# Kernel optimization log

Measured on AMD Instinct MI355X. Metric: run time of the kernel, lower is better.

## Reference

```python
import jax, jax.numpy as jnp
import numpy as np

BATCH, SEQ, FEAT, NUM_BINS = 64, 1024, 512, 32


def setup_inputs() -> dict:
    key = jax.random.key(0)
    k1, k2 = jax.random.split(key)
    features = jax.random.normal(k1, (BATCH, SEQ, FEAT), dtype=jnp.float32)
    # buffer: randn(input_dim, num_bins) / sqrt(input_dim)
    random_projection = jax.random.normal(k2, (FEAT, NUM_BINS), dtype=jnp.float32) / np.sqrt(FEAT)
    return {"features": features, "random_projection": random_projection}


def reference(features, random_projection):
    batch, seq, feat = features.shape
    x = features.reshape(-1, feat)  # [N, feat]
    N = x.shape[0]

    # RunningMeanStd.update from fresh state (mean=0, var=1, count=1e-4)
    eps_count = 1e-4
    batch_mean = x.mean(axis=0)
    batch_var = jnp.var(x, axis=0, ddof=1)  # torch.var is unbiased by default
    tot = eps_count + N
    delta = batch_mean  # - 0
    mean = delta * N / tot
    M2 = 1.0 * eps_count + batch_var * N + (delta ** 2) * eps_count * N / tot
    var = M2 / tot
    sigma = jnp.sqrt(var + 1e-8)

    normalized = (x - mean) / sigma
    projected = normalized @ random_projection  # [N, num_bins]
    bits = (projected > 0).astype(jnp.int64)
    pow2 = jnp.left_shift(jnp.int64(1), jnp.arange(NUM_BINS, dtype=jnp.int64))
    keys = (bits * pow2).sum(axis=-1)  # [N], values < 2^32

    # env_indices=None path: env = arange(N) % batch
    env = jnp.arange(N, dtype=jnp.int64) % batch
    combined = jnp.left_shift(env, 32) | keys  # unique (env, key) id

    # running occurrence count of each (env, key) in sample order i=0..N-1
    order = jnp.argsort(combined, stable=True)  # stable: preserves sample order within group
    s = combined[order]
    idx = jnp.arange(N, dtype=jnp.int64)
    is_start = jnp.concatenate([jnp.ones((1,), bool), s[1:] != s[:-1]])
    seg_start = jax.lax.cummax(jnp.where(is_start, idx, 0))
    occ = idx - seg_start + 1  # 1-based occurrence within group
    counts = jnp.zeros((N,), jnp.int64).at[order].set(occ)

    rewards = 1.0 / jnp.sqrt(counts.astype(features.dtype))
    return rewards.reshape(batch, seq, 1)
```

## Files before the change

kernel.cpp:

```cpp
#include <hip/hip_runtime.h>

using u16 = unsigned short;
using u64 = unsigned long long;
typedef short s16x8 __attribute__((ext_vector_type(8)));
typedef _Float16 f16x8 __attribute__((ext_vector_type(8)));
typedef unsigned short u16x4 __attribute__((ext_vector_type(4)));
typedef float f32x4 __attribute__((ext_vector_type(4)));

constexpr int BATCH = 64, SEQ = 1024, FEAT = 512, NBINS = 32;
constexpr int N = BATCH * SEQ;
constexpr int TAB = 131072;
constexpr unsigned TABMASK = TAB - 1;
constexpr u64 EMPTY = ~0ull;
constexpr double FXSCALE = 67108864.0;
constexpr int NSHADOW = 64;


constexpr size_t OFF_KEYS = 0;
constexpr size_t OFF_HEAD = 1048576;
constexpr size_t OFF_CNT = 1572864;
constexpr size_t OFF_SHAD = 2097152;
constexpr size_t OFF_QD = 2621504;
constexpr size_t OFF_CD = 2752576;
constexpr size_t OFF_CF = 2818304;
constexpr size_t OFF_SLOT = 2818432;
constexpr size_t OFF_NEXT = 3080576;
constexpr size_t OFF_QFRAG = 3342720;

__device__ inline u16 f2h(float f) {
  _Float16 h = (_Float16)f;
  return __builtin_bit_cast(u16, h);
}

__global__ __launch_bounds__(256, 4) void colstats_kernel(
    const float4* __restrict__ xv,
    u64* __restrict__ shad) {
  const int t = threadIdx.x;
  const int L = blockIdx.x * 256 + t;
  double s0 = 0, s1 = 0, s2 = 0, s3 = 0, q0 = 0, q1 = 0, q2 = 0, q3 = 0;
  for (int mm = 0; mm < 32; mm += 8) {
    float4 v[8];
#pragma unroll
    for (int u = 0; u < 8; u++) v[u] = xv[L + (mm + u) * 262144];
#pragma unroll
    for (int u = 0; u < 8; u++) {
      double a = (double)v[u].x, b = (double)v[u].y;
      double c = (double)v[u].z, d = (double)v[u].w;
      s0 += a; s1 += b; s2 += c; s3 += d;
      q0 += a * a; q1 += b * b; q2 += c * c; q3 += d * d;
    }
  }
  __shared__ double red[256 * 8];
  red[t * 8 + 0] = s0; red[t * 8 + 1] = s1; red[t * 8 + 2] = s2; red[t * 8 + 3] = s3;
  red[t * 8 + 4] = q0; red[t * 8 + 5] = q1; red[t * 8 + 6] = q2; red[t * 8 + 7] = q3;
  __syncthreads();
  if (t < 128) {
    double v[8];
#pragma unroll
    for (int u = 0; u < 8; u++) v[u] = red[t * 8 + u] + red[(t + 128) * 8 + u];
    const int c0 = 4 * t;
    u64* sh = shad + (size_t)(blockIdx.x & (NSHADOW - 1)) * 1024;
#pragma unroll
    for (int u = 0; u < 4; u++) {
      long long a = (long long)llrint(v[u] * FXSCALE);
      long long b = (long long)llrint(v[4 + u] * FXSCALE);
      atomicAdd(&sh[c0 + u], (u64)a);
      atomicAdd(&sh[512 + c0 + u], (u64)b);
    }
  }
}

__global__ __launch_bounds__(512) void finalize_kernel(
    const float* __restrict__ P,
    const u64* __restrict__ shad,
    double* __restrict__ Qd, u16* __restrict__ qfrag,
    double* __restrict__ cd, float* __restrict__ cf) {
  __shared__ double meanArr[FEAT];
  __shared__ double invArr[FEAT];
  __shared__ double part[16][NBINS];
  const int t = threadIdx.x;
  long long isum = 0, isumsq = 0;
  for (int sh = 0; sh < NSHADOW; sh++) {
    isum += (long long)shad[sh * 1024 + t];
    isumsq += (long long)shad[sh * 1024 + 512 + t];
  }
  const double Nd = (double)N;
  const double tot = 1e-4 + Nd;
  double s = (double)isum * (1.0 / FXSCALE);
  double ss = (double)isumsq * (1.0 / FXSCALE);
  double bm = s / Nd;
  double bv = (ss - s * s / Nd) / (Nd - 1.0);
  double mean = bm * Nd / tot;
  double M2 = 1e-4 + bv * Nd + bm * bm * 1e-4 * Nd / tot;
  double var = M2 / tot;
  double inv = 1.0 / sqrt(var + 1e-8);
  meanArr[t] = mean;
  invArr[t] = inv;
  const int ch = t >> 7, ks = (t >> 5) & 3, kg = (t >> 3) & 3, jlo = t & 7;
#pragma unroll
  for (int j = 0; j < NBINS; j++) {
    double qd = (double)P[t * NBINS + j] * inv;
    Qd[t * NBINS + j] = qd;
    const int lane = (j & 15) | (kg << 4);
    const int bt = j >> 4;
    qfrag[(size_t)((((ch * 4 + ks) * 2 + bt) * 64 + lane) * 8 + jlo)] =
        f2h((float)qd);
  }
  __syncthreads();
  {
    const int j = t & 31, g = t >> 5;
    double p = 0.0;
    for (int f = g * 32; f < g * 32 + 32; f++) {
      double qd = (double)P[f * NBINS + j] * invArr[f];
      p += meanArr[f] * qd;
    }
    part[g][j] = p;
  }
  __syncthreads();
  if (t < NBINS) {
    double c = 0.0;
    for (int g = 0; g < 16; g++) c += part[g][t];
    cd[t] = c;
    cf[t] = (float)c;
  }
}

constexpr float TAU = 4e-3f;
__global__ __launch_bounds__(256, 3) void project_kernel(
    const float4* __restrict__ xv, const float* __restrict__ feat,
    const u16* __restrict__ qfrag, const float* __restrict__ cf,
    const double* __restrict__ Qd, const double* __restrict__ cd,
    u64* __restrict__ keys_tab, int* __restrict__ head,
    unsigned* __restrict__ cnt, int* __restrict__ slot, int* __restrict__ nxt) {
  __shared__ __align__(16) u16 xh_lds[8192];
  __shared__ unsigned keyParts[64];
  const int t = threadIdx.x;
  const int rowBase = blockIdx.x * 64;
  const int lane = t & 63;
  const int w = t >> 6;
  if (t < 64) keyParts[t] = 0u;

  f32x4 acc0 = {0.f, 0.f, 0.f, 0.f};
  f32x4 acc1 = {0.f, 0.f, 0.f, 0.f};
  for (int ch = 0; ch < 4; ch++) {
    __syncthreads();
    s16x8 B[4][2];
#pragma unroll
    for (int ks = 0; ks < 4; ks++)
#pragma unroll
      for (int bt = 0; bt < 2; bt++)
        B[ks][bt] = *(const s16x8*)&qfrag[(size_t)((((ch * 4 + ks) * 2 + bt) * 64 + lane) * 8)];
#pragma unroll
    for (int kk = 0; kk < 8; kk++) {
      const int vi = t + kk * 256;
      const int r = vi >> 5, f4 = vi & 31;
      float4 v = xv[(size_t)(rowBase + r) * 128 + ch * 32 + f4];
      const int ks = f4 >> 3, kg = (f4 & 7) >> 1, j0 = (f4 & 1) * 4;
      const int lane_ = (r & 15) | (kg << 4);
      const int blk = ((r >> 4) * 4 + ks) * 64 + (lane_ ^ (((lane_ >> 4) & 3) << 1));
      u16x4 hv;
      hv[0] = f2h(v.x); hv[1] = f2h(v.y); hv[2] = f2h(v.z); hv[3] = f2h(v.w);
      *(u16x4*)&xh_lds[blk * 8 + j0] = hv;
    }
    __syncthreads();
#pragma unroll
    for (int ks = 0; ks < 4; ks++) {
      const int rblk = (w * 4 + ks) * 64 + (lane ^ (((lane >> 4) & 3) << 1));
      f16x8 a = __builtin_bit_cast(f16x8, *(const s16x8*)&xh_lds[rblk * 8]);
      acc0 = __builtin_amdgcn_mfma_f32_16x16x32_f16(
          a, __builtin_bit_cast(f16x8, B[ks][0]), acc0, 0, 0, 0);
      acc1 = __builtin_amdgcn_mfma_f32_16x16x32_f16(
          a, __builtin_bit_cast(f16x8, B[ks][1]), acc1, 0, 0, 0);
    }
  }
  const int colbin = lane & 15;
  float m0[4], m1[4];
  bool b0[4], b1[4];
  const float c0v = cf[colbin], c1v = cf[16 + colbin];
#pragma unroll
  for (int rg = 0; rg < 4; rg++) {
    m0[rg] = acc0[rg] - c0v;
    m1[rg] = acc1[rg] - c1v;
    b0[rg] = m0[rg] > 0.0f;
    b1[rg] = m1[rg] > 0.0f;
  }
#pragma unroll
  for (int bt = 0; bt < 2; bt++)
#pragma unroll
    for (int rg = 0; rg < 4; rg++) {
      const float mv = (bt == 0) ? m0[rg] : m1[rg];
      u64 mask = __ballot(fabsf(mv) < TAU);
      while (mask) {
        const int L = (int)__builtin_ctzll(mask);
        mask &= mask - 1;
        const int jj = bt * 16 + (L & 15);
        const int row = rowBase + w * 16 + (L >> 4) * 4 + rg;
        const float* xr = feat + (size_t)row * FEAT + lane * 8;
        const double* qp = Qd + (size_t)(lane * 8) * NBINS + jj;
        double p = 0.0;
#pragma unroll
        for (int u = 0; u < 8; u++) p = fma((double)xr[u], qp[u * NBINS], p);
#pragma unroll
        for (int off = 32; off > 0; off >>= 1) p += __shfl_xor(p, off, 64);
        const bool bit = p > cd[jj];
        if (lane == L) {
          if (bt == 0) b0[rg] = bit; else b1[rg] = bit;
        }
      }
    }
#pragma unroll
  for (int rg = 0; rg < 4; rg++) {
    const unsigned mybits = (b0[rg] ? (1u << colbin) : 0u) |
                            (b1[rg] ? (1u << (16 + colbin)) : 0u);
    atomicOr(&keyParts[w * 16 + (lane >> 4) * 4 + rg], mybits);
  }
  __syncthreads();
  if (t < 64) {
    const int i = rowBase + t;
    unsigned key = keyParts[t];
    u64 combined = (u64)key;
    unsigned idx = (unsigned)((combined * 0x9E3779B97F4A7C15ull) >> 47) & TABMASK;
    for (;;) {
      u64 prev = atomicCAS(&keys_tab[idx], EMPTY, combined);
      if (prev == EMPTY || prev == combined) break;
      idx = (idx + 1) & TABMASK;
    }
    slot[i] = (int)idx;
    atomicAdd(&cnt[idx], 1u);
    nxt[i] = atomicExch(&head[idx], i);
  }
}

__global__ __launch_bounds__(256) void count_kernel(
    const int* __restrict__ slot, const int* __restrict__ nxt,
    const int* __restrict__ head, const unsigned* __restrict__ cnt,
    float* __restrict__ out) {
  const int i = blockIdx.x * 256 + threadIdx.x;
  const int sl = slot[i];
  const unsigned c = cnt[sl];
  float r = 1.0f;
  if (c > 1u) {
    int j = head[sl];
    int occ = 1;
    while (j >= 0) {
      occ += (j < i) ? 1 : 0;
      j = nxt[j];
    }
    r = 1.0f / sqrtf((float)occ);
  }
  out[i] = r;
}

extern "C" void kernel_launch(void* const* d_in, const int* in_sizes, int n_in,
                              void* d_out, int out_size, void* d_ws, size_t ws_size,
                              hipStream_t stream) {
  const float4* xv = (const float4*)d_in[0];
  const float* feat = (const float*)d_in[0];
  const float* proj = (const float*)d_in[1];
  float* out = (float*)d_out;
  char* ws = (char*)d_ws;

  u64* keys_tab = (u64*)(ws + OFF_KEYS);
  int* head = (int*)(ws + OFF_HEAD);
  unsigned* cnt = (unsigned*)(ws + OFF_CNT);
  u64* shad = (u64*)(ws + OFF_SHAD);
  double* Qd = (double*)(ws + OFF_QD);
  double* cd = (double*)(ws + OFF_CD);
  float* cf = (float*)(ws + OFF_CF);
  int* slot = (int*)(ws + OFF_SLOT);
  int* nxt = (int*)(ws + OFF_NEXT);
  u16* qfrag = (u16*)(ws + OFF_QFRAG);

  (void)hipMemsetAsync(ws + OFF_KEYS, 0xFF, OFF_CNT - OFF_KEYS, stream);
  (void)hipMemsetAsync(ws + OFF_CNT, 0x00, OFF_QD - OFF_CNT, stream);

  colstats_kernel<<<1024, 256, 0, stream>>>(xv, shad);
  finalize_kernel<<<1, 512, 0, stream>>>(proj, shad, Qd, qfrag, cd, cf);
  project_kernel<<<N / 64, 256, 0, stream>>>(xv, feat, qfrag, cf, Qd, cd,
                                             keys_tab, head, cnt, slot, nxt);
  count_kernel<<<N / 256, 256, 0, stream>>>(slot, nxt, head, cnt, out);
}
```

Baseline: 269.4 us.

## Load MFMA A-fragments directly from global memory, drop LDS staging and block barriers

```diff
diff --git a/kernel.cpp b/kernel.cpp
--- a/kernel.cpp
+++ b/kernel.cpp
@@ -4,7 +4,6 @@
 using u64 = unsigned long long;
 typedef short s16x8 __attribute__((ext_vector_type(8)));
 typedef _Float16 f16x8 __attribute__((ext_vector_type(8)));
-typedef unsigned short u16x4 __attribute__((ext_vector_type(4)));
 typedef float f32x4 __attribute__((ext_vector_type(4)));
 
 constexpr int BATCH = 64, SEQ = 1024, FEAT = 512, NBINS = 32;
@@ -126,24 +125,22 @@
 }
 
 constexpr float TAU = 4e-3f;
-__global__ __launch_bounds__(256, 3) void project_kernel(
-    const float4* __restrict__ xv, const float* __restrict__ feat,
+__global__ __launch_bounds__(256) void project_kernel(
+    const float* __restrict__ feat,
     const u16* __restrict__ qfrag, const float* __restrict__ cf,
     const double* __restrict__ Qd, const double* __restrict__ cd,
     u64* __restrict__ keys_tab, int* __restrict__ head,
     unsigned* __restrict__ cnt, int* __restrict__ slot, int* __restrict__ nxt) {
-  __shared__ __align__(16) u16 xh_lds[8192];
-  __shared__ unsigned keyParts[64];
   const int t = threadIdx.x;
-  const int rowBase = blockIdx.x * 64;
   const int lane = t & 63;
   const int w = t >> 6;
-  if (t < 64) keyParts[t] = 0u;
+  const int rowBase = blockIdx.x * 64;
+  const int arow = rowBase + w * 16 + (lane & 15);
+  const float* xbase = feat + (size_t)arow * FEAT + (lane >> 4) * 8;
 
   f32x4 acc0 = {0.f, 0.f, 0.f, 0.f};
   f32x4 acc1 = {0.f, 0.f, 0.f, 0.f};
   for (int ch = 0; ch < 4; ch++) {
-    __syncthreads();
     s16x8 B[4][2];
 #pragma unroll
     for (int ks = 0; ks < 4; ks++)
@@ -151,22 +148,14 @@
       for (int bt = 0; bt < 2; bt++)
         B[ks][bt] = *(const s16x8*)&qfrag[(size_t)((((ch * 4 + ks) * 2 + bt) * 64 + lane) * 8)];
 #pragma unroll
-    for (int kk = 0; kk < 8; kk++) {
-      const int vi = t + kk * 256;
-      const int r = vi >> 5, f4 = vi & 31;
-      float4 v = xv[(size_t)(rowBase + r) * 128 + ch * 32 + f4];
-      const int ks = f4 >> 3, kg = (f4 & 7) >> 1, j0 = (f4 & 1) * 4;
-      const int lane_ = (r & 15) | (kg << 4);
-      const int blk = ((r >> 4) * 4 + ks) * 64 + (lane_ ^ (((lane_ >> 4) & 3) << 1));
-      u16x4 hv;
-      hv[0] = f2h(v.x); hv[1] = f2h(v.y); hv[2] = f2h(v.z); hv[3] = f2h(v.w);
-      *(u16x4*)&xh_lds[blk * 8 + j0] = hv;
-    }
-    __syncthreads();
-#pragma unroll
     for (int ks = 0; ks < 4; ks++) {
-      const int rblk = (w * 4 + ks) * 64 + (lane ^ (((lane >> 4) & 3) << 1));
-      f16x8 a = __builtin_bit_cast(f16x8, *(const s16x8*)&xh_lds[rblk * 8]);
+      float4 x0 = *(const float4*)(xbase + ch * 128 + ks * 32);
+      float4 x1 = *(const float4*)(xbase + ch * 128 + ks * 32 + 4);
+      f16x8 a;
+      a[0] = (_Float16)x0.x; a[1] = (_Float16)x0.y;
+      a[2] = (_Float16)x0.z; a[3] = (_Float16)x0.w;
+      a[4] = (_Float16)x1.x; a[5] = (_Float16)x1.y;
+      a[6] = (_Float16)x1.z; a[7] = (_Float16)x1.w;
       acc0 = __builtin_amdgcn_mfma_f32_16x16x32_f16(
           a, __builtin_bit_cast(f16x8, B[ks][0]), acc0, 0, 0, 0);
       acc1 = __builtin_amdgcn_mfma_f32_16x16x32_f16(
@@ -208,17 +197,22 @@
         }
       }
     }
-#pragma unroll
-  for (int rg = 0; rg < 4; rg++) {
-    const unsigned mybits = (b0[rg] ? (1u << colbin) : 0u) |
-                            (b1[rg] ? (1u << (16 + colbin)) : 0u);
-    atomicOr(&keyParts[w * 16 + (lane >> 4) * 4 + rg], mybits);
-  }
-  __syncthreads();
-  if (t < 64) {
-    const int i = rowBase + t;
-    unsigned key = keyParts[t];
-    u64 combined = (u64)key;
+  unsigned kb0 = (b0[0] ? (1u << colbin) : 0u) | (b1[0] ? (1u << (16 + colbin)) : 0u);
+  unsigned kb1 = (b0[1] ? (1u << colbin) : 0u) | (b1[1] ? (1u << (16 + colbin)) : 0u);
+  unsigned kb2 = (b0[2] ? (1u << colbin) : 0u) | (b1[2] ? (1u << (16 + colbin)) : 0u);
+  unsigned kb3 = (b0[3] ? (1u << colbin) : 0u) | (b1[3] ? (1u << (16 + colbin)) : 0u);
+#pragma unroll
+  for (int off = 1; off < 16; off <<= 1) {
+    kb0 |= __shfl_xor(kb0, off, 64);
+    kb1 |= __shfl_xor(kb1, off, 64);
+    kb2 |= __shfl_xor(kb2, off, 64);
+    kb3 |= __shfl_xor(kb3, off, 64);
+  }
+  const int sub = lane & 15;
+  if (sub < 4) {
+    const unsigned key = sub == 0 ? kb0 : sub == 1 ? kb1 : sub == 2 ? kb2 : kb3;
+    const int i = rowBase + w * 16 + (lane >> 4) * 4 + sub;
+    const u64 combined = (u64)key;
     unsigned idx = (unsigned)((combined * 0x9E3779B97F4A7C15ull) >> 47) & TABMASK;
     for (;;) {
       u64 prev = atomicCAS(&keys_tab[idx], EMPTY, combined);
@@ -276,7 +270,7 @@
 
   colstats_kernel<<<1024, 256, 0, stream>>>(xv, shad);
   finalize_kernel<<<1, 512, 0, stream>>>(proj, shad, Qd, qfrag, cd, cf);
-  project_kernel<<<N / 64, 256, 0, stream>>>(xv, feat, qfrag, cf, Qd, cd,
+  project_kernel<<<N / 64, 256, 0, stream>>>(feat, qfrag, cf, Qd, cd,
                                              keys_tab, head, cnt, slot, nxt);
   count_kernel<<<N / 256, 256, 0, stream>>>(slot, nxt, head, cnt, out);
 }
```

New measurement: 272.0 us. About the same (+0.9%).
